# Kernel optimization log

Hardware: AMD Instinct MI355X
Metric: run time of the kernel (lower is better)

The kernel has to match this reference:

```python
import jax, jax.numpy as jnp
import numpy as np

N_HEADS = 12


def setup_inputs() -> dict:
    key = jax.random.key(0)
    ks = jax.random.split(key, 5)
    B, T, D = 4, 2048, 768
    std = 1.0 / np.sqrt(D)
    return {
        "x": jax.random.normal(ks[0], (B, T, D), jnp.float32),
        "W_qkv": jax.random.normal(ks[1], (3 * D, D), jnp.float32) * std,
        "b_qkv": jax.random.normal(ks[2], (3 * D,), jnp.float32) * 0.02,
        "W_proj": jax.random.normal(ks[3], (D, D), jnp.float32) * std,
        "b_proj": jax.random.normal(ks[4], (D,), jnp.float32) * 0.02,
    }


def reference(x, W_qkv, b_qkv, W_proj, b_proj):
    # x: [B, T, D]; intended 3D path of the module (dropout = eval-mode identity)
    B, T, D = x.shape
    H = N_HEADS
    Dh = D // H
    scale = Dh ** -0.5
    qkv = x @ W_qkv.T + b_qkv                       # [B, T, 3D]
    qkv = qkv.reshape(B, T, 3, H, Dh)
    q = jnp.transpose(qkv[:, :, 0], (0, 2, 1, 3))    # [B, H, T, Dh]
    k = jnp.transpose(qkv[:, :, 1], (0, 2, 1, 3))
    v = jnp.transpose(qkv[:, :, 2], (0, 2, 1, 3))
    attn = jnp.einsum("bhqd,bhkd->bhqk", q, k) * scale  # [B, H, T, T]
    scores = jax.nn.softmax(attn, axis=-1)
    out = jnp.einsum("bhqk,bhkd->bhqd", scores, v)       # [B, H, T, Dh]
    out = jnp.transpose(out, (0, 2, 1, 3)).reshape(B, T, D)
    return out @ W_proj.T + b_proj
```

## Files before the change

### kernel.cpp

```cpp
#include <hip/hip_runtime.h>
#include <hip/hip_bf16.h>
#include <stdint.h>

typedef __bf16 bf16;
typedef __bf16 bf16x8 __attribute__((ext_vector_type(8)));
typedef __bf16 bf16x4 __attribute__((ext_vector_type(4)));
typedef short  s16x4  __attribute__((ext_vector_type(4)));
typedef short  s16x8  __attribute__((ext_vector_type(8)));
typedef float  f32x4  __attribute__((ext_vector_type(4)));

#define N_B 4
#define N_T 2048
#define N_D 768
#define N_H 12
#define N_DH 64
#define M_TOT (N_B * N_T)

__device__ __forceinline__ void async_copy16(const bf16* g, bf16* l) {
    __builtin_amdgcn_global_load_lds(
        (const __attribute__((address_space(1))) unsigned int*)g,
        (__attribute__((address_space(3))) unsigned int*)l,
        16, 0, 0);
}

__launch_bounds__(256)
__global__ void f2bf3(const float* __restrict__ a, bf16* __restrict__ oa, int na,
                      const float* __restrict__ b, bf16* __restrict__ ob, int nb,
                      const float* __restrict__ c, bf16* __restrict__ oc) {
    int i = (blockIdx.x * 256 + threadIdx.x) * 4;
    const float* src; bf16* dst;
    if (i < na)            { src = a; dst = oa; }
    else if (i < na + nb)  { src = b; dst = ob; i -= na; }
    else                   { src = c; dst = oc; i -= na + nb; }
    const float4 v = *(const float4*)(src + i);
    dst[i]     = (bf16)v.x;
    dst[i + 1] = (bf16)v.y;
    dst[i + 2] = (bf16)v.z;
    dst[i + 3] = (bf16)v.w;
}

#define GEMM_STAGE(P, K0)                                                      \
    _Pragma("unroll")                                                          \
    for (int jj = 0; jj < 4; jj++)                                             \
        async_copy16(Ab + (size_t)jj * 32 * KD + (K0), &lsA[P][(jj * 256 + t) * 8]); \
    _Pragma("unroll")                                                          \
    for (int jj = 0; jj < TN / 32; jj++)                                       \
        async_copy16(Bb + (size_t)jj * 32 * KD + (K0), &lsB[P][(jj * 256 + t) * 8]);

#define GEMM_CORE(A_PTR, B_PTR, KDIM, TN_)                                     \
    constexpr int KD = (KDIM);                                                 \
    constexpr int TN = (TN_);                                                  \
    constexpr int JJ = TN / 32;                                                \
    constexpr int NT = KD / 64;                                                \
    __shared__ bf16 lsA[2][128 * 64];                                          \
    __shared__ bf16 lsB[2][TN * 64];                                           \
    const int m0 = blockIdx.x * 128;                                           \
    const int n0 = blockIdx.y * TN;                                            \
    const int t  = threadIdx.x;                                                \
    const int w  = t >> 6, l = t & 63;                                         \
    const int wm = w & 1, wn = w >> 1;                                         \
    const int lr = l & 15, lq = l >> 4;                                        \
    f32x4 acc[4][JJ] = {};                                                     \
     \
    const int cs = (t & 7) ^ ((t >> 3) & 7);                                   \
    const bf16* Ab = (A_PTR) + (size_t)(m0 + (t >> 3)) * KD + cs * 8;          \
    const bf16* Bb = (B_PTR) + (size_t)(n0 + (t >> 3)) * KD + cs * 8;          \
    GEMM_STAGE(0, 0)                                                           \
    for (int t0 = 0; t0 < NT; t0++) {                                          \
        const int p = t0 & 1;                                                  \
        __syncthreads();                                                       \
        if (t0 + 1 < NT) { GEMM_STAGE(p ^ 1, (t0 + 1) * 64) }                  \
        _Pragma("unroll")                                                      \
        for (int ks = 0; ks < 2; ks++) {                                       \
            bf16x8 af[4], bfr[JJ];                                             \
            _Pragma("unroll")                                                  \
            for (int i = 0; i < 4; i++)                                        \
                af[i] = *(const bf16x8*)(&lsA[p][(wm * 64 + i * 16 + lr) * 64  \
                                         + (((ks * 4 + lq) ^ (lr & 7)) * 8)]); \
            _Pragma("unroll")                                                  \
            for (int j = 0; j < JJ; j++)                                       \
                bfr[j] = *(const bf16x8*)(&lsB[p][(wn * (TN / 2) + j * 16 + lr) * 64 \
                                          + (((ks * 4 + lq) ^ (lr & 7)) * 8)]); \
            _Pragma("unroll")                                                  \
            for (int i = 0; i < 4; i++)                                        \
                _Pragma("unroll")                                              \
                for (int j = 0; j < JJ; j++)                                   \
                    acc[i][j] = __builtin_amdgcn_mfma_f32_16x16x32_bf16(       \
                        af[i], bfr[j], acc[i][j], 0, 0, 0);                    \
        }                                                                      \
    }

__launch_bounds__(256)
__global__ void gemm_qkv(const bf16* __restrict__ X, const bf16* __restrict__ W,
                         const float* __restrict__ bias,
                         bf16* __restrict__ Q, bf16* __restrict__ K,
                         bf16* __restrict__ Vt) {
    GEMM_CORE(X, W, 768, 128)
    for (int i = 0; i < 4; i++) {
        const int rowb = m0 + wm * 64 + i * 16 + lq * 4;
        const int b_ = rowb >> 11, tt = rowb & 2047;
        for (int j = 0; j < 4; j++) {
            const int col   = n0 + wn * 64 + j * 16 + lr;
            const int which = col / 768;
            const int rem   = col - which * 768;
            const int h     = rem >> 6, d = rem & 63;
            const float bv  = bias[col];
            if (which == 2) {
                const int tile = tt >> 6, kl = tt & 63;
                const int ki = kl >> 4, lqv = (kl >> 2) & 3;
                const int idx = 32 * (ki & 1) + 8 * lqv + 4 * (ki >> 1);
                bf16x4 v4;
                for (int r2 = 0; r2 < 4; r2++) v4[r2] = (bf16)(acc[i][j][r2] + bv);
                *(bf16x4*)(Vt + ((size_t)((b_ * N_H + h) * 64 + d)) * 2048
                           + tile * 64 + idx) = v4;
            } else {
                bf16* dst = (which == 0) ? Q : K;
                const float sc = (which == 0) ? 0.18033688f : 1.0f;
                for (int r2 = 0; r2 < 4; r2++)
                    dst[(size_t)(((b_ * N_H + h) << 11) + tt + r2) * 64 + d] =
                        (bf16)((acc[i][j][r2] + bv) * sc);
            }
        }
    }
}

__launch_bounds__(256)
__global__ void gemm_proj(const bf16* __restrict__ O, const bf16* __restrict__ W,
                          const float* __restrict__ bias, float* __restrict__ out) {
    GEMM_CORE(O, W, 768, 64)
    for (int i = 0; i < 4; i++) {
        const int rowb = m0 + wm * 64 + i * 16 + lq * 4;
        for (int j = 0; j < JJ; j++) {
            const int col  = n0 + wn * (TN / 2) + j * 16 + lr;
            const float bv = bias[col];
            for (int r = 0; r < 4; r++)
                out[(size_t)(rowb + r) * 768 + col] = acc[i][j][r] + bv;
        }
    }
}

__launch_bounds__(256, 3)
__global__ void attn(const bf16* __restrict__ Q, const bf16* __restrict__ K,
                     const bf16* __restrict__ Vt, bf16* __restrict__ O) {
    __shared__ bf16 lsK[2][64 * 64];
    __shared__ bf16 lsV[2][64 * 64];
    const int bid = blockIdx.x;
    const int xcd = bid & 7, slot = bid >> 3;
    const int bh  = xcd + 8 * (slot >> 4);
    const int qt  = slot & 15;
    const int t = threadIdx.x, w = t >> 6, l = t & 63;
    const int lr = l & 15, lq = l >> 4;
    const bf16* Qh  = Q  + (size_t)bh * N_T * 64;
    const bf16* Kh  = K  + (size_t)bh * N_T * 64;
    const bf16* Vth = Vt + (size_t)bh * 64 * N_T;
    const int q0 = qt * 128 + w * 32;

    bf16x8 qf[2][2];
    #pragma unroll
    for (int qg = 0; qg < 2; qg++)
        #pragma unroll
        for (int ks = 0; ks < 2; ks++)
            qf[qg][ks] = *(const bf16x8*)(Qh + (size_t)(q0 + qg * 16 + lr) * 64
                                          + ks * 32 + lq * 8);

    f32x4 oacc[2][4] = {};
    f32x4 lacc[2]    = {};
    const bf16x8 ones8 = {(bf16)1.f, (bf16)1.f, (bf16)1.f, (bf16)1.f,
                          (bf16)1.f, (bf16)1.f, (bf16)1.f, (bf16)1.f};

    #pragma unroll
    for (int j = 0; j < 2; j++) {
        const int u   = t + j * 256;
        const int row = u >> 3;
        const int scn = (u & 7) ^ (row & 7);
        async_copy16(Kh  + (size_t)row * 64 + scn * 8,   lsK[0] + u * 8);
        async_copy16(Vth + (size_t)row * 2048 + scn * 8, lsV[0] + u * 8);
    }

    for (int kt = 0; kt < 32; kt++) {
        const int cur = kt & 1;
        __syncthreads();

        if (kt < 31) {
            #pragma unroll
            for (int j = 0; j < 2; j++) {
                const int u   = t + j * 256;
                const int row = u >> 3;
                const int scn = (u & 7) ^ (row & 7);
                async_copy16(Kh + (size_t)((kt + 1) * 64 + row) * 64 + scn * 8,
                             lsK[cur ^ 1] + u * 8);
                async_copy16(Vth + (size_t)row * 2048 + (kt + 1) * 64 + scn * 8,
                             lsV[cur ^ 1] + u * 8);
            }
        }

        bf16x8 kf[2][4];
        #pragma unroll
        for (int ks = 0; ks < 2; ks++)
            #pragma unroll
            for (int ki = 0; ki < 4; ki++) {
                const int row = ki * 16 + lr;
                kf[ks][ki] = *(const bf16x8*)(lsK[cur] + row * 64
                                              + ((ks * 4 + lq) ^ (lr & 7)) * 8);
            }

        bf16x8 pbf[2][2];
        #pragma unroll
        for (int qg = 0; qg < 2; qg++) {
            f32x4 sacc[4] = {};
            __builtin_amdgcn_s_setprio(1);
            #pragma unroll
            for (int ks = 0; ks < 2; ks++)
                #pragma unroll
                for (int ki = 0; ki < 4; ki++)
                    sacc[ki] = __builtin_amdgcn_mfma_f32_16x16x32_bf16(
                        kf[ks][ki], qf[qg][ks], sacc[ki], 0, 0, 0);
            __builtin_amdgcn_s_setprio(0);
            #pragma unroll
            for (int ks = 0; ks < 2; ks++) {
                bf16x8 pb;
                #pragma unroll
                for (int r = 0; r < 4; r++) {
                    pb[r]     = (bf16)exp2f(sacc[ks][r]);
                    pb[4 + r] = (bf16)exp2f(sacc[ks + 2][r]);
                }
                pbf[qg][ks] = pb;
            }
        }

        __builtin_amdgcn_s_setprio(1);
        #pragma unroll
        for (int ks = 0; ks < 2; ks++)
            #pragma unroll
            for (int dj = 0; dj < 4; dj++) {
                const int row  = dj * 16 + lr;
                const int unit = (4 * ks + lq) ^ (lr & 7);
                bf16x8 vf = *(const bf16x8*)(lsV[cur] + row * 64 + unit * 8);
                #pragma unroll
                for (int qg = 0; qg < 2; qg++)
                    oacc[qg][dj] = __builtin_amdgcn_mfma_f32_16x16x32_bf16(
                        vf, pbf[qg][ks], oacc[qg][dj], 0, 0, 0);
            }
        #pragma unroll
        for (int qg = 0; qg < 2; qg++)
            #pragma unroll
            for (int ks = 0; ks < 2; ks++)
                lacc[qg] = __builtin_amdgcn_mfma_f32_16x16x32_bf16(
                    ones8, pbf[qg][ks], lacc[qg], 0, 0, 0);
        __builtin_amdgcn_s_setprio(0);
    }

    const int b = bh / N_H, h = bh - b * N_H;
    #pragma unroll
    for (int qg = 0; qg < 2; qg++) {
        const float inv_l = 1.0f / lacc[qg][0];
        const int tok = q0 + qg * 16 + lr;
        bf16* Ob = O + ((size_t)b * N_T + tok) * N_D + h * 64;
        #pragma unroll
        for (int dj = 0; dj < 4; dj++) {
            bf16x4 o4;
            #pragma unroll
            for (int r = 0; r < 4; r++) o4[r] = (bf16)(oacc[qg][dj][r] * inv_l);
            *(bf16x4*)(Ob + dj * 16 + lq * 4) = o4;
        }
    }
}

extern "C" void kernel_launch(void* const* d_in, const int* in_sizes, int n_in,
                              void* d_out, int out_size, void* d_ws, size_t ws_size,
                              hipStream_t stream) {
    const float* x      = (const float*)d_in[0];
    const float* W_qkv  = (const float*)d_in[1];
    const float* b_qkv  = (const float*)d_in[2];
    const float* W_proj = (const float*)d_in[3];
    const float* b_proj = (const float*)d_in[4];
    float* out = (float*)d_out;

    char* ws = (char*)d_ws;
    const size_t n_x  = (size_t)M_TOT * N_D;
    const size_t n_wq = (size_t)3 * N_D * N_D;
    const size_t n_wp = (size_t)N_D * N_D;
    const size_t sz_qkv = (size_t)N_B * N_H * N_T * N_DH * sizeof(bf16);

    bf16* xb  = (bf16*)(ws);                 ws += n_x * sizeof(bf16);
    bf16* Wqb = (bf16*)(ws);                 ws += n_wq * sizeof(bf16);
    bf16* Wpb = (bf16*)(ws);                 ws += n_wp * sizeof(bf16);
    bf16* Qb  = (bf16*)(ws);                 ws += sz_qkv;
    bf16* Kb  = (bf16*)(ws);                 ws += sz_qkv;
    bf16* Vtb = (bf16*)(ws);                 ws += sz_qkv;
    bf16* Ob  = (bf16*)(ws);

    dim3 blk(256);
    f2bf3<<<dim3((int)((n_x + n_wq + n_wp) / 1024)), blk, 0, stream>>>(
        x, xb, (int)n_x, W_qkv, Wqb, (int)n_wq, W_proj, Wpb);

    gemm_qkv<<<dim3(M_TOT / 128, 2304 / 128), blk, 0, stream>>>(xb, Wqb, b_qkv, Qb, Kb, Vtb);
    attn<<<dim3(768), dim3(256), 0, stream>>>(Qb, Kb, Vtb, Ob);
    gemm_proj<<<dim3(M_TOT / 128, 768 / 64), blk, 0, stream>>>(Ob, Wpb, b_proj, out);
}
```

Measured before the change: 221.1 us.

## Load K/V fragments directly from global memory in attention, drop LDS staging

The attention kernel no longer stages K and V tiles through double-buffered LDS with async copies and barriers; each wave reads its K and V MFMA fragments straight from global memory, relying on cache reuse across the four waves. This removes the per-tile __syncthreads and LDS traffic, and frees LDS, which may allow more blocks per CU. The cost is four times the global or L2 load traffic per block, with no explicit prefetch to hide latency. The fp32-to-bf16 cast kernel also writes its four outputs as one vector store.

```diff
diff --git a/kernel.cpp b/kernel.cpp
--- a/kernel.cpp
+++ b/kernel.cpp
@@ -33,10 +33,9 @@
     else if (i < na + nb)  { src = b; dst = ob; i -= na; }
     else                   { src = c; dst = oc; i -= na + nb; }
     const float4 v = *(const float4*)(src + i);
-    dst[i]     = (bf16)v.x;
-    dst[i + 1] = (bf16)v.y;
-    dst[i + 2] = (bf16)v.z;
-    dst[i + 3] = (bf16)v.w;
+    bf16x4 o;
+    o[0] = (bf16)v.x; o[1] = (bf16)v.y; o[2] = (bf16)v.z; o[3] = (bf16)v.w;
+    *(bf16x4*)(dst + i) = o;
 }
 
 #define GEMM_STAGE(P, K0)                                                      \
@@ -61,7 +60,6 @@
     const int wm = w & 1, wn = w >> 1;                                         \
     const int lr = l & 15, lq = l >> 4;                                        \
     f32x4 acc[4][JJ] = {};                                                     \
-     \
     const int cs = (t & 7) ^ ((t >> 3) & 7);                                   \
     const bf16* Ab = (A_PTR) + (size_t)(m0 + (t >> 3)) * KD + cs * 8;          \
     const bf16* Bb = (B_PTR) + (size_t)(n0 + (t >> 3)) * KD + cs * 8;          \
@@ -142,8 +140,6 @@
 __launch_bounds__(256, 3)
 __global__ void attn(const bf16* __restrict__ Q, const bf16* __restrict__ K,
                      const bf16* __restrict__ Vt, bf16* __restrict__ O) {
-    __shared__ bf16 lsK[2][64 * 64];
-    __shared__ bf16 lsV[2][64 * 64];
     const int bid = blockIdx.x;
     const int xcd = bid & 7, slot = bid >> 3;
     const int bh  = xcd + 8 * (slot >> 4);
@@ -168,41 +164,17 @@
     const bf16x8 ones8 = {(bf16)1.f, (bf16)1.f, (bf16)1.f, (bf16)1.f,
                           (bf16)1.f, (bf16)1.f, (bf16)1.f, (bf16)1.f};
 
-    #pragma unroll
-    for (int j = 0; j < 2; j++) {
-        const int u   = t + j * 256;
-        const int row = u >> 3;
-        const int scn = (u & 7) ^ (row & 7);
-        async_copy16(Kh  + (size_t)row * 64 + scn * 8,   lsK[0] + u * 8);
-        async_copy16(Vth + (size_t)row * 2048 + scn * 8, lsV[0] + u * 8);
-    }
+    const bf16* Kbase = Kh  + (size_t)lr * 64   + lq * 8;
+    const bf16* Vbase = Vth + (size_t)lr * 2048 + lq * 8;
 
     for (int kt = 0; kt < 32; kt++) {
-        const int cur = kt & 1;
-        __syncthreads();
-
-        if (kt < 31) {
-            #pragma unroll
-            for (int j = 0; j < 2; j++) {
-                const int u   = t + j * 256;
-                const int row = u >> 3;
-                const int scn = (u & 7) ^ (row & 7);
-                async_copy16(Kh + (size_t)((kt + 1) * 64 + row) * 64 + scn * 8,
-                             lsK[cur ^ 1] + u * 8);
-                async_copy16(Vth + (size_t)row * 2048 + (kt + 1) * 64 + scn * 8,
-                             lsV[cur ^ 1] + u * 8);
-            }
-        }
-
         bf16x8 kf[2][4];
         #pragma unroll
         for (int ks = 0; ks < 2; ks++)
             #pragma unroll
-            for (int ki = 0; ki < 4; ki++) {
-                const int row = ki * 16 + lr;
-                kf[ks][ki] = *(const bf16x8*)(lsK[cur] + row * 64
-                                              + ((ks * 4 + lq) ^ (lr & 7)) * 8);
-            }
+            for (int ki = 0; ki < 4; ki++)
+                kf[ks][ki] = *(const bf16x8*)(Kbase + (size_t)kt * 4096
+                                              + ki * 1024 + ks * 32);
 
         bf16x8 pbf[2][2];
         #pragma unroll
@@ -233,9 +205,8 @@
         for (int ks = 0; ks < 2; ks++)
             #pragma unroll
             for (int dj = 0; dj < 4; dj++) {
-                const int row  = dj * 16 + lr;
-                const int unit = (4 * ks + lq) ^ (lr & 7);
-                bf16x8 vf = *(const bf16x8*)(lsV[cur] + row * 64 + unit * 8);
+                bf16x8 vf = *(const bf16x8*)(Vbase + (size_t)dj * 32768
+                                             + kt * 64 + ks * 32);
                 #pragma unroll
                 for (int qg = 0; qg < 2; qg++)
                     oacc[qg][dj] = __builtin_amdgcn_mfma_f32_16x16x32_bf16(
```

Measured after the change: 321.3 us. +45.4%, slower.
